# Kernel optimization log

Hardware: AMD Instinct MI355X
Metric: run time of the kernel (lower is better)

The kernel has to match this reference:

```python
import jax, jax.numpy as jnp
import numpy as np

N, D = 2048, 1024
OUT = 65536
S = 16384  # number of LSH-selected neurons


def setup_inputs() -> dict:
    key = jax.random.key(0)
    k1, k2, k3, k4 = jax.random.split(key, 4)
    x = jax.random.normal(k1, (N, D), dtype=jnp.float32)
    # original init: uniform(-1, 1) weights, zero bias; use randn-scale weights per spec
    weight = jax.random.normal(k2, (OUT, D), dtype=jnp.float32)
    bias = jax.random.normal(k3, (OUT,), dtype=jnp.float32)
    sample_ids = jax.random.randint(k4, (S,), 0, OUT, dtype=jnp.int64)
    return {"x": x, "weight": weight, "bias": bias, "sample_ids": sample_ids}


def reference(x, weight, bias, sample_ids):
    # Gather selected neuron rows (F.embedding equivalent)
    sample_weights = weight[sample_ids]          # [S, D]
    sample_bias = bias[sample_ids]               # [S]
    # x @ W_sel.T + b_sel  -> [N, S]
    sample_logits = jnp.einsum('nd,sd->ns', x, sample_weights) + sample_bias
    return sample_logits
```

## Files before the change

### kernel.cpp

```cpp
#include <hip/hip_runtime.h>
#include <stdint.h>


typedef __bf16 bf16x8 __attribute__((ext_vector_type(8)));
typedef float f32x4 __attribute__((ext_vector_type(4)));

#define BM 128
#define BN 128
#define BK 64

__device__ __forceinline__ ushort f2bf(float f) {
  union { float f; uint32_t u; } c; c.f = f;
  uint32_t u = c.u;
  return (ushort)((u + 0x7FFFu + ((u >> 16) & 1u)) >> 16);
}

__global__ __launch_bounds__(256) void prep_kernel(
    const float* __restrict__ x, const float* __restrict__ W,
    const float* __restrict__ bias, const int* __restrict__ ids,
    ushort* __restrict__ Wg, ushort* __restrict__ xb,
    float* __restrict__ biasg, int D, int S) {
  const int t = threadIdx.x;
  const int gblocks = S >> 3;
  if ((int)blockIdx.x < gblocks) {
    const int s0 = blockIdx.x << 3;
    if (t < 8) biasg[s0 + t] = bias[ids[s0 + t]];
#pragma unroll
    for (int r = 0; r < 8; ++r) {
      const int s = s0 + r;
      const int id = ids[s];
      float4 v = ((const float4*)(W + (size_t)id * D))[t];
      ushort4 o;
      o.x = f2bf(v.x); o.y = f2bf(v.y); o.z = f2bf(v.z); o.w = f2bf(v.w);
      ((ushort4*)(Wg + (size_t)s * D))[t] = o;
    }
  } else {
    const int i = (blockIdx.x - gblocks) * 256 + t;
    float4 v = ((const float4*)x)[i];
    ushort4 o;
    o.x = f2bf(v.x); o.y = f2bf(v.y); o.z = f2bf(v.z); o.w = f2bf(v.w);
    ((ushort4*)xb)[i] = o;
  }
}

__device__ __forceinline__ void load_lds16(const void* g, void* l) {
  __builtin_amdgcn_global_load_lds(
      (const __attribute__((address_space(1))) void*)g,
      (__attribute__((address_space(3))) void*)l, 16, 0, 0);
}

__device__ __forceinline__ const ushort* frag_ptr(const ushort* base, int row,
                                                  int c) {
  return base + row * BK + (((c ^ (row & 7)) << 3));
}

__global__ __launch_bounds__(256) void gemm_bt_bias(
    const ushort* __restrict__ A, const ushort* __restrict__ B,
    const float* __restrict__ biasg, float* __restrict__ C,
    int M, int S, int K) {
  __shared__ __align__(16) ushort As[BM * BK];
  __shared__ __align__(16) ushort Bs[BN * BK];

  const int tid  = threadIdx.x;
  const int lane = tid & 63;
  const int wave = tid >> 6;
  const int bn = blockIdx.x;
  const int bm = blockIdx.y;

  const int wm = (wave >> 1) * 64;
  const int wn = (wave & 1) * 64;
  const int quad = lane >> 4;
  const int l16  = lane & 15;

  const int srow = tid >> 3;
  const int scol = (((tid & 7) ^ (srow & 7)) << 3);
  const ushort* Ag = A + (size_t)(bm * BM + srow) * K + scol;
  const ushort* Bg = B + (size_t)(bn * BN + srow) * K + scol;
  ushort* Asl = As + tid * 8;
  ushort* Bsl = Bs + tid * 8;

  f32x4 acc[4][4] = {};

  for (int kt = 0; kt < K; kt += BK) {
#pragma unroll
    for (int i = 0; i < 4; ++i) {
      load_lds16(Ag + (size_t)(i * 32) * K, Asl + i * 32 * BK);
      load_lds16(Bg + (size_t)(i * 32) * K, Bsl + i * 32 * BK);
    }
    Ag += BK; Bg += BK;
    __syncthreads();

#pragma unroll
    for (int ks = 0; ks < BK; ks += 32) {
      const int c0 = (ks >> 3) + quad;
      bf16x8 af[4], bq[4];
#pragma unroll
      for (int i = 0; i < 4; ++i)
        af[i] = *(const bf16x8*)frag_ptr(As, wm + i * 16 + l16, c0);
#pragma unroll
      for (int j = 0; j < 4; ++j)
        bq[j] = *(const bf16x8*)frag_ptr(Bs, wn + j * 16 + l16, c0);
#pragma unroll
      for (int i = 0; i < 4; ++i)
#pragma unroll
        for (int j = 0; j < 4; ++j)
          acc[i][j] = __builtin_amdgcn_mfma_f32_16x16x32_bf16(
              af[i], bq[j], acc[i][j], 0, 0, 0);
    }
    __syncthreads();
  }

  const int row0 = bm * BM + wm + quad * 4;
  const int col0 = bn * BN + wn + l16;
#pragma unroll
  for (int j = 0; j < 4; ++j) {
    const int col = col0 + j * 16;
    const float bv = biasg[col];
#pragma unroll
    for (int i = 0; i < 4; ++i) {
#pragma unroll
      for (int r = 0; r < 4; ++r) {
        C[(size_t)(row0 + i * 16 + r) * S + col] = acc[i][j][r] + bv;
      }
    }
  }
}

extern "C" void kernel_launch(void* const* d_in, const int* in_sizes, int n_in,
                              void* d_out, int out_size, void* d_ws, size_t ws_size,
                              hipStream_t stream) {
  const float* x    = (const float*)d_in[0];
  const float* W    = (const float*)d_in[1];
  const float* bias = (const float*)d_in[2];
  const int*   ids  = (const int*)d_in[3];
  float* out = (float*)d_out;

  const int OUTN = in_sizes[2];
  const int S    = in_sizes[3];
  const int D    = in_sizes[1] / OUTN;
  const int N    = in_sizes[0] / D;

  ushort* Wg = (ushort*)d_ws;
  ushort* xb = (ushort*)((char*)d_ws + (size_t)S * D * sizeof(ushort));
  float* biasg = (float*)((char*)d_ws + (size_t)S * D * sizeof(ushort)
                          + (size_t)N * D * sizeof(ushort));

  const int gather_blocks = S / 8;
  const int conv_blocks = (N * D) / 1024;
  prep_kernel<<<gather_blocks + conv_blocks, 256, 0, stream>>>(
      x, W, bias, ids, Wg, xb, biasg, D, S);

  dim3 grid(S / BN, N / BM);
  gemm_bt_bias<<<grid, 256, 0, stream>>>(xb, Wg, biasg, out, N, S, D);
}
```

Baseline: 433.2 us.

## Switch to 32x32x16 MFMA tiles and grouped block rasterization

Measured after the change: 435.1 us. No clear change (+0.4%).

```diff
diff --git a/kernel.cpp b/kernel.cpp
--- a/kernel.cpp
+++ b/kernel.cpp
@@ -3,7 +3,7 @@
 
 
 typedef __bf16 bf16x8 __attribute__((ext_vector_type(8)));
-typedef float f32x4 __attribute__((ext_vector_type(4)));
+typedef float f32x16 __attribute__((ext_vector_type(16)));
 
 #define BM 128
 #define BN 128
@@ -64,13 +64,19 @@
   const int tid  = threadIdx.x;
   const int lane = tid & 63;
   const int wave = tid >> 6;
-  const int bn = blockIdx.x;
-  const int bm = blockIdx.y;
+
+  const int num_bm = M / BM;
+  const int pid = blockIdx.x;
+  const int group_sz = num_bm * 8;
+  const int g = pid / group_sz;
+  const int r = pid % group_sz;
+  const int bn = g * 8 + (r & 7);
+  const int bm = r >> 3;
 
   const int wm = (wave >> 1) * 64;
   const int wn = (wave & 1) * 64;
-  const int quad = lane >> 4;
-  const int l16  = lane & 15;
+  const int l31  = lane & 31;
+  const int half = lane >> 5;
 
   const int srow = tid >> 3;
   const int scol = (((tid & 7) ^ (srow & 7)) << 3);
@@ -79,7 +85,7 @@
   ushort* Asl = As + tid * 8;
   ushort* Bsl = Bs + tid * 8;
 
-  f32x4 acc[4][4] = {};
+  f32x16 acc[2][2] = {};
 
   for (int kt = 0; kt < K; kt += BK) {
 #pragma unroll
@@ -91,36 +97,37 @@
     __syncthreads();
 
 #pragma unroll
-    for (int ks = 0; ks < BK; ks += 32) {
-      const int c0 = (ks >> 3) + quad;
-      bf16x8 af[4], bq[4];
+    for (int ks = 0; ks < BK; ks += 16) {
+      const int c0 = (ks >> 3) + half;
+      bf16x8 af[2], bq[2];
 #pragma unroll
-      for (int i = 0; i < 4; ++i)
-        af[i] = *(const bf16x8*)frag_ptr(As, wm + i * 16 + l16, c0);
+      for (int i = 0; i < 2; ++i)
+        af[i] = *(const bf16x8*)frag_ptr(As, wm + i * 32 + l31, c0);
 #pragma unroll
-      for (int j = 0; j < 4; ++j)
-        bq[j] = *(const bf16x8*)frag_ptr(Bs, wn + j * 16 + l16, c0);
+      for (int j = 0; j < 2; ++j)
+        bq[j] = *(const bf16x8*)frag_ptr(Bs, wn + j * 32 + l31, c0);
 #pragma unroll
-      for (int i = 0; i < 4; ++i)
+      for (int i = 0; i < 2; ++i)
 #pragma unroll
-        for (int j = 0; j < 4; ++j)
-          acc[i][j] = __builtin_amdgcn_mfma_f32_16x16x32_bf16(
+        for (int j = 0; j < 2; ++j)
+          acc[i][j] = __builtin_amdgcn_mfma_f32_32x32x16_bf16(
               af[i], bq[j], acc[i][j], 0, 0, 0);
     }
     __syncthreads();
   }
 
-  const int row0 = bm * BM + wm + quad * 4;
-  const int col0 = bn * BN + wn + l16;
+  const int row_base = bm * BM + wm + 4 * half;
+  const int col_base = bn * BN + wn + l31;
 #pragma unroll
-  for (int j = 0; j < 4; ++j) {
-    const int col = col0 + j * 16;
+  for (int j = 0; j < 2; ++j) {
+    const int col = col_base + j * 32;
     const float bv = biasg[col];
 #pragma unroll
-    for (int i = 0; i < 4; ++i) {
+    for (int i = 0; i < 2; ++i) {
 #pragma unroll
-      for (int r = 0; r < 4; ++r) {
-        C[(size_t)(row0 + i * 16 + r) * S + col] = acc[i][j][r] + bv;
+      for (int reg = 0; reg < 16; ++reg) {
+        const int row = row_base + i * 32 + (reg & 3) + 8 * (reg >> 2);
+        C[(size_t)row * S + col] = acc[i][j][reg] + bv;
       }
     }
   }
@@ -150,6 +157,6 @@
   prep_kernel<<<gather_blocks + conv_blocks, 256, 0, stream>>>(
       x, W, bias, ids, Wg, xb, biasg, D, S);
 
-  dim3 grid(S / BN, N / BM);
-  gemm_bt_bias<<<grid, 256, 0, stream>>>(xb, Wg, biasg, out, N, S, D);
+  const int total_blocks = (S / BN) * (N / BM);
+  gemm_bt_bias<<<total_blocks, 256, 0, stream>>>(xb, Wg, biasg, out, N, S, D);
 }
```
